# Kernel tuning notes

Hardware: AMD Instinct MI355X
Metric: run time of the kernel (lower is better)

The kernel has to match this reference:

```python
import jax, jax.numpy as jnp
import numpy as np
import math

B, S, D, H = 4, 2048, 1024, 16
HD = D // H  # 64
MOD_DIMS = [("text", 768, 2048), ("image", 1024, 1024), ("audio", 512, 1500), ("video", 2048, 512)]
M = len(MOD_DIMS)
WIN, DEPTH = 3, 8


def _cantor_routes():
    coords = []
    for i in range(M):
        x = i / max(1, M - 1)
        x = max(1e-06, min(x, 1.0 - 1e-06))
        val, f = 0.0, 0.5
        for _ in range(DEPTH):
            x *= 3.0
            d = int(x)
            x -= d
            if d == 2:
                val += f
            f *= 0.5
        coords.append(val)
    c = np.asarray(coords, dtype=np.float32)
    dist = np.abs(c[:, None] - c[None, :])
    # topk smallest distances (stable tie-break like torch ascending sort)
    return np.argsort(dist, axis=1, kind="stable")[:, :WIN]

ROUTES = jnp.asarray(_cantor_routes())


def setup_inputs() -> dict:
    key = jax.random.key(0)
    ks = iter(jax.random.split(key, 32))
    inp = {}
    for name, dim, sl in MOD_DIMS:
        inp[name] = jax.random.normal(next(ks), (B, sl, dim), dtype=jnp.float32)
        inp[f"W_{name}"] = jax.random.normal(next(ks), (D, dim), dtype=jnp.float32) / math.sqrt(dim)
        inp[f"b_{name}"] = jnp.zeros((D,), dtype=jnp.float32)
    inp["mod_emb"] = jax.random.normal(next(ks), (M, D), dtype=jnp.float32) * 0.02
    for nm in ("q", "k", "v", "o"):
        inp[f"W{nm}"] = jax.random.normal(next(ks), (D, D), dtype=jnp.float32) / math.sqrt(D)
        inp[f"b{nm}"] = jnp.zeros((D,), dtype=jnp.float32)
    inp["temperature"] = jnp.asarray(0.07, dtype=jnp.float32)
    return inp


def reference(text, image, audio, video, W_text, b_text, W_image, b_image,
              W_audio, b_audio, W_video, b_video, mod_emb, Wq, bq, Wk, bk,
              Wv, bv, Wo, bo, temperature):
    xs = [text, image, audio, video]
    Ws = [W_text, W_image, W_audio, W_video]
    bs = [b_text, b_image, b_audio, b_video]
    projected = []
    for i in range(M):
        p = xs[i] @ Ws[i].T + bs[i] + mod_emb[i]          # [B, s_i, D]
        p = jnp.pad(p, ((0, 0), (0, S - p.shape[1]), (0, 0)))
        projected.append(p)
    stacked = jnp.stack(projected, axis=1)                # [B, M, S, D]

    def heads(x, W, b):
        return (x @ W.T + b).reshape(B, M, S, H, HD).transpose(0, 3, 1, 2, 4)  # [B,H,M,S,HD]

    Q = heads(stacked, Wq, bq)
    K = heads(stacked, Wk, bk)
    V = heads(stacked, Wv, bv)

    Kn = K[:, :, ROUTES]
    Vn = V[:, :, ROUTES]
    scores = jnp.einsum('bhmsd,bhmwsd->bhmsw', Q, Kn) / (math.sqrt(HD) * jnp.abs(temperature))
    attn = jax.nn.softmax(scores, axis=-1)                # dropout is identity at eval
    out = jnp.einsum('bhmsw,bhmwsd->bhmsd', attn, Vn)     # [B,H,M,S,HD]
    fused = out.mean(axis=2)                              # [B,H,S,HD]
    fused = fused.transpose(0, 2, 1, 3).reshape(B, S, D)
    return fused @ Wo.T + bo
```

## Files before the change

### kernel.cpp

```cpp
#include <hip/hip_runtime.h>

typedef unsigned short u16;
typedef __bf16 bf16x8 __attribute__((ext_vector_type(8)));
typedef u16   u16x8  __attribute__((ext_vector_type(8)));
typedef u16   u16x4  __attribute__((ext_vector_type(4)));
typedef float f32x4  __attribute__((ext_vector_type(4)));

#define RPB 5084
#define SL0 2048
#define SL1 1024
#define SL2 1500
#define SL3 512

__device__ __forceinline__ u16 f2bf(float f) {
  union { float f; unsigned u; } x; x.f = f;
  unsigned u = x.u;
  u += 0x7fffu + ((u >> 16) & 1u);
  return (u16)(u >> 16);
}
__device__ __forceinline__ float bf2f(u16 h) {
  union { unsigned u; float f; } x; x.u = ((unsigned)h) << 16;
  return x.f;
}
__device__ __forceinline__ void gll16(const u16* g, u16* l) {
  __builtin_amdgcn_global_load_lds(
      (const __attribute__((address_space(1))) void*)g,
      (__attribute__((address_space(3))) void*)l, 16, 0, 0);
}

#define NSEG 12
struct CvtSegs {
  const float* src[NSEG];
  u16*         dst[NSEG];
  int          blk_end[NSEG];
  int          blk_base[NSEG];
};
__global__ __launch_bounds__(256) void cvt_multi(CvtSegs segs) {
  int blk = blockIdx.x, seg = 0;
#pragma unroll
  for (int s = 0; s < NSEG; ++s) if (blk >= segs.blk_end[s]) seg = s + 1;
  const float* src = segs.src[seg];
  u16* dst = segs.dst[seg];
  int i = (blk - segs.blk_base[seg]) * 1024 + threadIdx.x * 4;
  f32x4 v = *(const f32x4*)(src + i);
  u16x4 o;
  o[0] = f2bf(v[0]); o[1] = f2bf(v[1]); o[2] = f2bf(v[2]); o[3] = f2bf(v[3]);
  *(u16x4*)(dst + i) = o;
}

template<int STORE_F32>
__global__ __launch_bounds__(256) void gemm_lds(
    const u16* __restrict__ A,
    const u16* __restrict__ B0, const u16* __restrict__ B1, const u16* __restrict__ B2,
    const float* __restrict__ c0, const float* __restrict__ c1, const float* __restrict__ c2,
    void* __restrict__ Cout, int Mr, int K, int ldc)
{
  __shared__ u16 lA[128 * 32];
  __shared__ u16 lB[128 * 32];
  const int tid  = threadIdx.x;
  const int lane = tid & 63;
  const int wave = tid >> 6;
  const int wr   = (wave >> 1) * 64;
  const int wc   = (wave & 1) * 64;
  const int row0 = blockIdx.y * 128;

  const int wsel = blockIdx.x >> 3;
  const int colL = (blockIdx.x & 7) * 128;
  const u16*   Bw   = (wsel == 0) ? B0 : (wsel == 1) ? B1 : B2;
  const float* bias = (wsel == 0) ? c0 : (wsel == 1) ? c1 : c2;

  const int sr  = wave * 32 + (lane >> 2);
  const int sc  = (lane & 3) * 8;
  int ra0 = row0 + sr;      if (ra0 >= Mr) ra0 = Mr - 1;
  int ra1 = row0 + sr + 16; if (ra1 >= Mr) ra1 = Mr - 1;
  const u16* pA0 = A + (size_t)ra0 * K + sc;
  const u16* pA1 = A + (size_t)ra1 * K + sc;
  const u16* pB0 = Bw + (size_t)(colL + sr) * K + sc;
  const u16* pB1 = pB0 + (size_t)16 * K;
  u16* dA0 = &lA[(wave * 32) * 32];
  u16* dA1 = &lA[(wave * 32 + 16) * 32];
  u16* dB0 = &lB[(wave * 32) * 32];
  u16* dB1 = &lB[(wave * 32 + 16) * 32];

  f32x4 acc[4][4];
#pragma unroll
  for (int i = 0; i < 4; ++i)
#pragma unroll
    for (int j = 0; j < 4; ++j) acc[i][j] = f32x4{0.f, 0.f, 0.f, 0.f};

  const int fr = lane & 15;
  const int fk = (lane >> 4) * 8;

  for (int k0 = 0; k0 < K; k0 += 32) {
    __syncthreads();
    gll16(pA0 + k0, dA0);
    gll16(pA1 + k0, dA1);
    gll16(pB0 + k0, dB0);
    gll16(pB1 + k0, dB1);
    __syncthreads();

    bf16x8 af[4], bfr[4];
#pragma unroll
    for (int i = 0; i < 4; ++i)
      af[i] = *(const bf16x8*)&lA[(wr + i * 16 + fr) * 32 + fk];
#pragma unroll
    for (int j = 0; j < 4; ++j)
      bfr[j] = *(const bf16x8*)&lB[(wc + j * 16 + fr) * 32 + fk];
#pragma unroll
    for (int i = 0; i < 4; ++i)
#pragma unroll
      for (int j = 0; j < 4; ++j)
        acc[i][j] = __builtin_amdgcn_mfma_f32_16x16x32_bf16(af[i], bfr[j], acc[i][j], 0, 0, 0);
  }

  const int fc = lane & 15;
  const int rq = (lane >> 4) * 4;
#pragma unroll
  for (int i = 0; i < 4; ++i) {
#pragma unroll
    for (int j = 0; j < 4; ++j) {
      const int cl = wc + j * 16 + fc;
      const float badd = bias[colL + cl];
      const int gc = blockIdx.x * 128 + cl;
#pragma unroll
      for (int reg = 0; reg < 4; ++reg) {
        int gr = row0 + wr + i * 16 + rq + reg;
        if (gr < Mr) {
          float v = acc[i][j][reg] + badd;
          if (STORE_F32) ((float*)Cout)[(size_t)gr * ldc + gc] = v;
          else           ((u16*)Cout)[(size_t)gr * ldc + gc] = f2bf(v);
        }
      }
    }
  }
}

struct ProjSegs {
  const u16*   A[4];
  const u16*   Bw[4];
  const float* b0[4];
  const float* b1[4];
  int Mr[4], K[4], sl[4], obase[4];
  int blk_end[4];
};
__global__ __launch_bounds__(256) void gemm_proj_all(ProjSegs ps, u16* __restrict__ Cout) {
  int blk = blockIdx.x, seg = 0;
#pragma unroll
  for (int s = 0; s < 3; ++s) if (blk >= ps.blk_end[s]) seg = s + 1;
  const int base  = seg ? ps.blk_end[seg - 1] : 0;
  const int local = blk - base;
  const int row0  = (local >> 3) * 128;
  const int col0  = (local & 7) * 128;
  const int Mr = ps.Mr[seg], K = ps.K[seg], sl = ps.sl[seg], obase = ps.obase[seg];
  const u16* A  = ps.A[seg];
  const u16* Bw = ps.Bw[seg];
  const float* bias0 = ps.b0[seg];
  const float* bias1 = ps.b1[seg];

  __shared__ u16 lA[128 * 32];
  __shared__ u16 lB[128 * 32];
  const int tid  = threadIdx.x;
  const int lane = tid & 63;
  const int wave = tid >> 6;
  const int wr   = (wave >> 1) * 64;
  const int wc   = (wave & 1) * 64;

  const int sr  = wave * 32 + (lane >> 2);
  const int sc  = (lane & 3) * 8;
  int ra0 = row0 + sr;      if (ra0 >= Mr) ra0 = Mr - 1;
  int ra1 = row0 + sr + 16; if (ra1 >= Mr) ra1 = Mr - 1;
  const u16* pA0 = A + (size_t)ra0 * K + sc;
  const u16* pA1 = A + (size_t)ra1 * K + sc;
  const u16* pB0 = Bw + (size_t)(col0 + sr) * K + sc;
  const u16* pB1 = pB0 + (size_t)16 * K;
  u16* dA0 = &lA[(wave * 32) * 32];
  u16* dA1 = &lA[(wave * 32 + 16) * 32];
  u16* dB0 = &lB[(wave * 32) * 32];
  u16* dB1 = &lB[(wave * 32 + 16) * 32];

  f32x4 acc[4][4];
#pragma unroll
  for (int i = 0; i < 4; ++i)
#pragma unroll
    for (int j = 0; j < 4; ++j) acc[i][j] = f32x4{0.f, 0.f, 0.f, 0.f};

  const int fr = lane & 15;
  const int fk = (lane >> 4) * 8;

  for (int k0 = 0; k0 < K; k0 += 32) {
    __syncthreads();
    gll16(pA0 + k0, dA0);
    gll16(pA1 + k0, dA1);
    gll16(pB0 + k0, dB0);
    gll16(pB1 + k0, dB1);
    __syncthreads();

    bf16x8 af[4], bfr[4];
#pragma unroll
    for (int i = 0; i < 4; ++i)
      af[i] = *(const bf16x8*)&lA[(wr + i * 16 + fr) * 32 + fk];
#pragma unroll
    for (int j = 0; j < 4; ++j)
      bfr[j] = *(const bf16x8*)&lB[(wc + j * 16 + fr) * 32 + fk];
#pragma unroll
    for (int i = 0; i < 4; ++i)
#pragma unroll
      for (int j = 0; j < 4; ++j)
        acc[i][j] = __builtin_amdgcn_mfma_f32_16x16x32_bf16(af[i], bfr[j], acc[i][j], 0, 0, 0);
  }

  const int fc = lane & 15;
  const int rq = (lane >> 4) * 4;
#pragma unroll
  for (int i = 0; i < 4; ++i) {
#pragma unroll
    for (int j = 0; j < 4; ++j) {
      const int c = col0 + wc + j * 16 + fc;
      const float badd = bias0[c] + bias1[c];
#pragma unroll
      for (int reg = 0; reg < 4; ++reg) {
        int gr = row0 + wr + i * 16 + rq + reg;
        if (gr < Mr) {
          int bb = gr / sl, ss = gr - bb * sl;
          Cout[(size_t)(bb * RPB + obase + ss) * 1024 + c] = f2bf(acc[i][j][reg] + badd);
        }
      }
    }
  }
}

__global__ __launch_bounds__(256) void attn_fuse(
    const u16* __restrict__ QKV,
    u16* __restrict__ fused,
    const float* __restrict__ bq, const float* __restrict__ bk, const float* __restrict__ bv,
    const float* __restrict__ temp_ptr)
{
  const int ROUTE[4][3] = {{0,1,2},{0,1,2},{2,3,0},{3,2,0}};
  const int SLm[4]  = {SL0, SL1, SL2, SL3};
  const int OFFS[4] = {0, 2048, 3072, 4572};
  const int tid  = threadIdx.x;
  const int lane = tid & 63;
  const int wave = tid >> 6;
  const int bs   = blockIdx.x * 2 + (wave >> 1);
  const int s    = bs & 2047;
  const int b    = bs >> 11;
  const int h    = (wave & 1) * 8 + (lane >> 3);
  const int sub  = lane & 7;
  const int dbase = h * 64 + sub * 8;
  const float scale = 1.0f / (8.0f * fabsf(temp_ptr[0]));

  float acc[8];
#pragma unroll
  for (int i = 0; i < 8; ++i) acc[i] = 0.f;

#pragma unroll
  for (int m = 0; m < 4; ++m) {
    float qf[8];
    if (s < SLm[m]) {
      u16x8 q8 = *(const u16x8*)(QKV + ((size_t)(b * RPB + OFFS[m] + s)) * 3072 + dbase);
#pragma unroll
      for (int i = 0; i < 8; ++i) qf[i] = bf2f(q8[i]);
    } else {
#pragma unroll
      for (int i = 0; i < 8; ++i) qf[i] = bq[dbase + i];
    }
    float sc[3];
#pragma unroll
    for (int w = 0; w < 3; ++w) {
      const int r = ROUTE[m][w];
      float d = 0.f;
      if (s < SLm[r]) {
        u16x8 k8 = *(const u16x8*)(QKV + ((size_t)(b * RPB + OFFS[r] + s)) * 3072 + 1024 + dbase);
#pragma unroll
        for (int i = 0; i < 8; ++i) d += qf[i] * bf2f(k8[i]);
      } else {
#pragma unroll
        for (int i = 0; i < 8; ++i) d += qf[i] * bk[dbase + i];
      }
      d += __shfl_xor(d, 1, 64);
      d += __shfl_xor(d, 2, 64);
      d += __shfl_xor(d, 4, 64);
      sc[w] = d * scale;
    }
    float mx = fmaxf(sc[0], fmaxf(sc[1], sc[2]));
    float e0 = __expf(sc[0] - mx), e1 = __expf(sc[1] - mx), e2 = __expf(sc[2] - mx);
    float inv = 1.0f / (e0 + e1 + e2);
    float ws[3] = {e0 * inv, e1 * inv, e2 * inv};
#pragma unroll
    for (int w = 0; w < 3; ++w) {
      const int r = ROUTE[m][w];
      if (s < SLm[r]) {
        u16x8 v8 = *(const u16x8*)(QKV + ((size_t)(b * RPB + OFFS[r] + s)) * 3072 + 2048 + dbase);
#pragma unroll
        for (int i = 0; i < 8; ++i) acc[i] += ws[w] * bf2f(v8[i]);
      } else {
#pragma unroll
        for (int i = 0; i < 8; ++i) acc[i] += ws[w] * bv[dbase + i];
      }
    }
  }
  u16x8 o;
#pragma unroll
  for (int i = 0; i < 8; ++i) o[i] = f2bf(acc[i] * 0.25f);
  *(u16x8*)(fused + (size_t)bs * 1024 + dbase) = o;
}

extern "C" void kernel_launch(void* const* d_in, const int* in_sizes, int n_in,
                              void* d_out, int out_size, void* d_ws, size_t ws_size,
                              hipStream_t stream) {
  const int B = 4, S = 2048, D = 1024;
  const int SL[4]   = {SL0, SL1, SL2, SL3};
  const int DIM[4]  = {768, 1024, 512, 2048};
  const int OFFS[4] = {0, 2048, 3072, 4572};

  const float* x[4]  = {(const float*)d_in[0], (const float*)d_in[3], (const float*)d_in[6], (const float*)d_in[9]};
  const float* Wm[4] = {(const float*)d_in[1], (const float*)d_in[4], (const float*)d_in[7], (const float*)d_in[10]};
  const float* bm[4] = {(const float*)d_in[2], (const float*)d_in[5], (const float*)d_in[8], (const float*)d_in[11]};
  const float* mod_emb = (const float*)d_in[12];
  const float* Wq = (const float*)d_in[13]; const float* bq = (const float*)d_in[14];
  const float* Wk = (const float*)d_in[15]; const float* bk = (const float*)d_in[16];
  const float* Wv = (const float*)d_in[17]; const float* bv = (const float*)d_in[18];
  const float* Wo = (const float*)d_in[19]; const float* bo = (const float*)d_in[20];
  const float* temp = (const float*)d_in[21];

  const int RROWS = B * RPB;
  const size_t stackedB = ((size_t)RROWS * D * 2 + 255) / 256 * 256;
  const size_t qkvB     = ((size_t)RROWS * 3 * D * 2 + 255) / 256 * 256;
  const size_t wB       = ((size_t)D * D * 2 + 255) / 256 * 256;
  size_t wmB[4];
  for (int m = 0; m < 4; ++m) wmB[m] = ((size_t)D * DIM[m] * 2 + 255) / 256 * 256;
  const size_t need = stackedB + qkvB + 4 * wB + wmB[0] + wmB[1] + wmB[2] + wmB[3];
  if (ws_size < need) return;

  char* p = (char*)d_ws;
  u16* stacked = (u16*)p;  p += stackedB;
  char* qkvbase = p;
  u16* qkv     = (u16*)p;  p += qkvB;
  u16* wqb     = (u16*)p;  p += wB;
  u16* wkb     = (u16*)p;  p += wB;
  u16* wvb     = (u16*)p;  p += wB;
  u16* wob     = (u16*)p;  p += wB;
  u16* wmb[4];
  for (int m = 0; m < 4; ++m) { wmb[m] = (u16*)p; p += wmB[m]; }
  u16* fusedb  = stacked;

  u16* xb[4];
  {
    char* q = qkvbase;
    for (int m = 0; m < 4; ++m) {
      xb[m] = (u16*)q;
      q += ((size_t)B * SL[m] * DIM[m] * 2 + 255) / 256 * 256;
    }
  }

  {
    CvtSegs cs;
    const float* srcs[NSEG] = {x[0], x[1], x[2], x[3], Wm[0], Wm[1], Wm[2], Wm[3], Wq, Wk, Wv, Wo};
    u16* dsts[NSEG] = {xb[0], xb[1], xb[2], xb[3], wmb[0], wmb[1], wmb[2], wmb[3], wqb, wkb, wvb, wob};
    int ns[NSEG];
    for (int m = 0; m < 4; ++m) ns[m] = B * SL[m] * DIM[m];
    for (int m = 0; m < 4; ++m) ns[4 + m] = D * DIM[m];
    for (int i = 0; i < 4; ++i) ns[8 + i] = D * D;
    int base = 0;
    for (int i = 0; i < NSEG; ++i) {
      cs.src[i] = srcs[i]; cs.dst[i] = dsts[i];
      cs.blk_base[i] = base;
      base += (ns[i] + 1023) / 1024;
      cs.blk_end[i] = base;
    }
    cvt_multi<<<base, 256, 0, stream>>>(cs);
  }

  {
    ProjSegs ps;
    int base = 0;
    for (int m = 0; m < 4; ++m) {
      int Mr = B * SL[m];
      ps.A[m] = xb[m]; ps.Bw[m] = wmb[m];
      ps.b0[m] = bm[m]; ps.b1[m] = mod_emb + m * D;
      ps.Mr[m] = Mr; ps.K[m] = DIM[m]; ps.sl[m] = SL[m]; ps.obase[m] = OFFS[m];
      base += 8 * ((Mr + 127) / 128);
      ps.blk_end[m] = base;
    }
    gemm_proj_all<<<base, 256, 0, stream>>>(ps, stacked);
  }

  {
    dim3 grid(24, (RROWS + 127) / 128);
    gemm_lds<0><<<grid, 256, 0, stream>>>(stacked, wqb, wkb, wvb, bq, bk, bv,
                                          qkv, RROWS, D, 3 * D);
  }

  attn_fuse<<<(B * S) / 2, 256, 0, stream>>>(qkv, fusedb, bq, bk, bv, temp);

  {
    dim3 grid(8, (B * S) / 128);
    gemm_lds<1><<<grid, 256, 0, stream>>>(fusedb, wob, wob, wob, bo, bo, bo,
                                          d_out, B * S, D, D);
  }
}
```

Baseline: 508.4 us.

## Widen GEMM K-step to 64, dedupe attention QKV loads, reorder projection blocks

```diff
diff --git a/kernel.cpp b/kernel.cpp
--- a/kernel.cpp
+++ b/kernel.cpp
@@ -48,6 +48,7 @@
   *(u16x4*)(dst + i) = o;
 }
 
+
 template<int STORE_F32>
 __global__ __launch_bounds__(256) void gemm_lds(
     const u16* __restrict__ A,
@@ -55,8 +56,8 @@
     const float* __restrict__ c0, const float* __restrict__ c1, const float* __restrict__ c2,
     void* __restrict__ Cout, int Mr, int K, int ldc)
 {
-  __shared__ u16 lA[128 * 32];
-  __shared__ u16 lB[128 * 32];
+  __shared__ u16 lA0[128 * 32], lA1[128 * 32];
+  __shared__ u16 lB0[128 * 32], lB1[128 * 32];
   const int tid  = threadIdx.x;
   const int lane = tid & 63;
   const int wave = tid >> 6;
@@ -77,10 +78,10 @@
   const u16* pA1 = A + (size_t)ra1 * K + sc;
   const u16* pB0 = Bw + (size_t)(colL + sr) * K + sc;
   const u16* pB1 = pB0 + (size_t)16 * K;
-  u16* dA0 = &lA[(wave * 32) * 32];
-  u16* dA1 = &lA[(wave * 32 + 16) * 32];
-  u16* dB0 = &lB[(wave * 32) * 32];
-  u16* dB1 = &lB[(wave * 32 + 16) * 32];
+  u16* dA0a = &lA0[(wave * 32) * 32];      u16* dA1a = &lA0[(wave * 32 + 16) * 32];
+  u16* dA0b = &lA1[(wave * 32) * 32];      u16* dA1b = &lA1[(wave * 32 + 16) * 32];
+  u16* dB0a = &lB0[(wave * 32) * 32];      u16* dB1a = &lB0[(wave * 32 + 16) * 32];
+  u16* dB0b = &lB1[(wave * 32) * 32];      u16* dB1b = &lB1[(wave * 32 + 16) * 32];
 
   f32x4 acc[4][4];
 #pragma unroll
@@ -91,21 +92,32 @@
   const int fr = lane & 15;
   const int fk = (lane >> 4) * 8;
 
-  for (int k0 = 0; k0 < K; k0 += 32) {
+  for (int k0 = 0; k0 < K; k0 += 64) {
     __syncthreads();
-    gll16(pA0 + k0, dA0);
-    gll16(pA1 + k0, dA1);
-    gll16(pB0 + k0, dB0);
-    gll16(pB1 + k0, dB1);
+    gll16(pA0 + k0, dA0a);       gll16(pA1 + k0, dA1a);
+    gll16(pB0 + k0, dB0a);       gll16(pB1 + k0, dB1a);
+    gll16(pA0 + k0 + 32, dA0b);  gll16(pA1 + k0 + 32, dA1b);
+    gll16(pB0 + k0 + 32, dB0b);  gll16(pB1 + k0 + 32, dB1b);
     __syncthreads();
 
     bf16x8 af[4], bfr[4];
 #pragma unroll
     for (int i = 0; i < 4; ++i)
-      af[i] = *(const bf16x8*)&lA[(wr + i * 16 + fr) * 32 + fk];
+      af[i] = *(const bf16x8*)&lA0[(wr + i * 16 + fr) * 32 + fk];
 #pragma unroll
     for (int j = 0; j < 4; ++j)
-      bfr[j] = *(const bf16x8*)&lB[(wc + j * 16 + fr) * 32 + fk];
+      bfr[j] = *(const bf16x8*)&lB0[(wc + j * 16 + fr) * 32 + fk];
+#pragma unroll
+    for (int i = 0; i < 4; ++i)
+#pragma unroll
+      for (int j = 0; j < 4; ++j)
+        acc[i][j] = __builtin_amdgcn_mfma_f32_16x16x32_bf16(af[i], bfr[j], acc[i][j], 0, 0, 0);
+#pragma unroll
+    for (int i = 0; i < 4; ++i)
+      af[i] = *(const bf16x8*)&lA1[(wr + i * 16 + fr) * 32 + fk];
+#pragma unroll
+    for (int j = 0; j < 4; ++j)
+      bfr[j] = *(const bf16x8*)&lB1[(wc + j * 16 + fr) * 32 + fk];
 #pragma unroll
     for (int i = 0; i < 4; ++i)
 #pragma unroll
@@ -157,8 +169,8 @@
   const float* bias0 = ps.b0[seg];
   const float* bias1 = ps.b1[seg];
 
-  __shared__ u16 lA[128 * 32];
-  __shared__ u16 lB[128 * 32];
+  __shared__ u16 lA0[128 * 32], lA1[128 * 32];
+  __shared__ u16 lB0[128 * 32], lB1[128 * 32];
   const int tid  = threadIdx.x;
   const int lane = tid & 63;
   const int wave = tid >> 6;
@@ -173,10 +185,10 @@
   const u16* pA1 = A + (size_t)ra1 * K + sc;
   const u16* pB0 = Bw + (size_t)(col0 + sr) * K + sc;
   const u16* pB1 = pB0 + (size_t)16 * K;
-  u16* dA0 = &lA[(wave * 32) * 32];
-  u16* dA1 = &lA[(wave * 32 + 16) * 32];
-  u16* dB0 = &lB[(wave * 32) * 32];
-  u16* dB1 = &lB[(wave * 32 + 16) * 32];
+  u16* dA0a = &lA0[(wave * 32) * 32];      u16* dA1a = &lA0[(wave * 32 + 16) * 32];
+  u16* dA0b = &lA1[(wave * 32) * 32];      u16* dA1b = &lA1[(wave * 32 + 16) * 32];
+  u16* dB0a = &lB0[(wave * 32) * 32];      u16* dB1a = &lB0[(wave * 32 + 16) * 32];
+  u16* dB0b = &lB1[(wave * 32) * 32];      u16* dB1b = &lB1[(wave * 32 + 16) * 32];
 
   f32x4 acc[4][4];
 #pragma unroll
@@ -187,21 +199,32 @@
   const int fr = lane & 15;
   const int fk = (lane >> 4) * 8;
 
-  for (int k0 = 0; k0 < K; k0 += 32) {
+  for (int k0 = 0; k0 < K; k0 += 64) {
     __syncthreads();
-    gll16(pA0 + k0, dA0);
-    gll16(pA1 + k0, dA1);
-    gll16(pB0 + k0, dB0);
-    gll16(pB1 + k0, dB1);
+    gll16(pA0 + k0, dA0a);       gll16(pA1 + k0, dA1a);
+    gll16(pB0 + k0, dB0a);       gll16(pB1 + k0, dB1a);
+    gll16(pA0 + k0 + 32, dA0b);  gll16(pA1 + k0 + 32, dA1b);
+    gll16(pB0 + k0 + 32, dB0b);  gll16(pB1 + k0 + 32, dB1b);
     __syncthreads();
 
     bf16x8 af[4], bfr[4];
 #pragma unroll
     for (int i = 0; i < 4; ++i)
-      af[i] = *(const bf16x8*)&lA[(wr + i * 16 + fr) * 32 + fk];
+      af[i] = *(const bf16x8*)&lA0[(wr + i * 16 + fr) * 32 + fk];
 #pragma unroll
     for (int j = 0; j < 4; ++j)
-      bfr[j] = *(const bf16x8*)&lB[(wc + j * 16 + fr) * 32 + fk];
+      bfr[j] = *(const bf16x8*)&lB0[(wc + j * 16 + fr) * 32 + fk];
+#pragma unroll
+    for (int i = 0; i < 4; ++i)
+#pragma unroll
+      for (int j = 0; j < 4; ++j)
+        acc[i][j] = __builtin_amdgcn_mfma_f32_16x16x32_bf16(af[i], bfr[j], acc[i][j], 0, 0, 0);
+#pragma unroll
+    for (int i = 0; i < 4; ++i)
+      af[i] = *(const bf16x8*)&lA1[(wr + i * 16 + fr) * 32 + fk];
+#pragma unroll
+    for (int j = 0; j < 4; ++j)
+      bfr[j] = *(const bf16x8*)&lB1[(wc + j * 16 + fr) * 32 + fk];
 #pragma unroll
     for (int i = 0; i < 4; ++i)
 #pragma unroll
@@ -249,34 +272,39 @@
   const int dbase = h * 64 + sub * 8;
   const float scale = 1.0f / (8.0f * fabsf(temp_ptr[0]));
 
+  float qf[4][8], kf[4][8], vf[4][8];
+#pragma unroll
+  for (int r = 0; r < 4; ++r) {
+    if (s < SLm[r]) {
+      const u16* base = QKV + ((size_t)(b * RPB + OFFS[r] + s)) * 3072 + dbase;
+      u16x8 q8 = *(const u16x8*)(base);
+      u16x8 k8 = *(const u16x8*)(base + 1024);
+      u16x8 v8 = *(const u16x8*)(base + 2048);
+#pragma unroll
+      for (int i = 0; i < 8; ++i) {
+        qf[r][i] = bf2f(q8[i]); kf[r][i] = bf2f(k8[i]); vf[r][i] = bf2f(v8[i]);
+      }
+    } else {
+#pragma unroll
+      for (int i = 0; i < 8; ++i) {
+        qf[r][i] = bq[dbase + i]; kf[r][i] = bk[dbase + i]; vf[r][i] = bv[dbase + i];
+      }
+    }
+  }
+
   float acc[8];
 #pragma unroll
   for (int i = 0; i < 8; ++i) acc[i] = 0.f;
 
 #pragma unroll
   for (int m = 0; m < 4; ++m) {
-    float qf[8];
-    if (s < SLm[m]) {
-      u16x8 q8 = *(const u16x8*)(QKV + ((size_t)(b * RPB + OFFS[m] + s)) * 3072 + dbase);
-#pragma unroll
-      for (int i = 0; i < 8; ++i) qf[i] = bf2f(q8[i]);
-    } else {
-#pragma unroll
-      for (int i = 0; i < 8; ++i) qf[i] = bq[dbase + i];
-    }
     float sc[3];
 #pragma unroll
     for (int w = 0; w < 3; ++w) {
       const int r = ROUTE[m][w];
       float d = 0.f;
-      if (s < SLm[r]) {
-        u16x8 k8 = *(const u16x8*)(QKV + ((size_t)(b * RPB + OFFS[r] + s)) * 3072 + 1024 + dbase);
-#pragma unroll
-        for (int i = 0; i < 8; ++i) d += qf[i] * bf2f(k8[i]);
-      } else {
-#pragma unroll
-        for (int i = 0; i < 8; ++i) d += qf[i] * bk[dbase + i];
-      }
+#pragma unroll
+      for (int i = 0; i < 8; ++i) d += qf[m][i] * kf[r][i];
       d += __shfl_xor(d, 1, 64);
       d += __shfl_xor(d, 2, 64);
       d += __shfl_xor(d, 4, 64);
@@ -289,14 +317,8 @@
 #pragma unroll
     for (int w = 0; w < 3; ++w) {
       const int r = ROUTE[m][w];
-      if (s < SLm[r]) {
-        u16x8 v8 = *(const u16x8*)(QKV + ((size_t)(b * RPB + OFFS[r] + s)) * 3072 + 2048 + dbase);
-#pragma unroll
-        for (int i = 0; i < 8; ++i) acc[i] += ws[w] * bf2f(v8[i]);
-      } else {
-#pragma unroll
-        for (int i = 0; i < 8; ++i) acc[i] += ws[w] * bv[dbase + i];
-      }
+#pragma unroll
+      for (int i = 0; i < 8; ++i) acc[i] += ws[w] * vf[r][i];
     }
   }
   u16x8 o;
@@ -372,15 +394,17 @@
   }
 
   {
+    const int ord[4] = {3, 1, 0, 2};
     ProjSegs ps;
     int base = 0;
-    for (int m = 0; m < 4; ++m) {
+    for (int i = 0; i < 4; ++i) {
+      int m = ord[i];
       int Mr = B * SL[m];
-      ps.A[m] = xb[m]; ps.Bw[m] = wmb[m];
-      ps.b0[m] = bm[m]; ps.b1[m] = mod_emb + m * D;
-      ps.Mr[m] = Mr; ps.K[m] = DIM[m]; ps.sl[m] = SL[m]; ps.obase[m] = OFFS[m];
+      ps.A[i] = xb[m]; ps.Bw[i] = wmb[m];
+      ps.b0[i] = bm[m]; ps.b1[i] = mod_emb + m * D;
+      ps.Mr[i] = Mr; ps.K[i] = DIM[m]; ps.sl[i] = SL[m]; ps.obase[i] = OFFS[m];
       base += 8 * ((Mr + 127) / 128);
-      ps.blk_end[m] = base;
+      ps.blk_end[i] = base;
     }
     gemm_proj_all<<<base, 256, 0, stream>>>(ps, stacked);
   }
```

Result: faster. 458.2 us (-9.9%).
